# Kernel tuning notes

Hardware: AMD Instinct MI355X
Metric: run time of the kernel (lower is better)

Reference implementation:

```python
import jax, jax.numpy as jnp
import numpy as np
from jax import lax


def setup_inputs() -> dict:
    key = jax.random.key(0)
    ks = jax.random.split(key, 20)
    B, D, T = 1024, 256, 128
    H, O = 256, 64
    f32 = jnp.float32
    rn = lambda k, shape, sc: jax.random.normal(k, shape, f32) * sc
    ru = lambda k, shape: jax.random.uniform(k, shape, f32)
    return {
        "x": jax.random.normal(ks[0], (B, D, T), f32),
        "W_in": rn(ks[1], (H, D), 1.0 / np.sqrt(D)),
        "b_in": rn(ks[2], (H,), 0.02),
        "beta1": ru(ks[3], (H,)),
        "thr1": ru(ks[4], (H,)),
        "W_h": rn(ks[5], (H, H), 1.0 / np.sqrt(H)),
        "b_h": rn(ks[6], (H,), 0.02),
        "beta2": ru(ks[7], (H,)),
        "thr2": ru(ks[8], (H,)),
        "W_h1": rn(ks[9], (H, H), 1.0 / np.sqrt(H)),
        "b_h1": rn(ks[10], (H,), 0.02),
        "W_f": rn(ks[11], (O, H), 1.0 / np.sqrt(H)),
        "b_f": rn(ks[12], (O,), 0.02),
        "beta_f": ru(ks[13], (O,)),
        "W_a": rn(ks[14], (O, H), 1.0 / np.sqrt(H)),
        "b_a": rn(ks[15], (O,), 0.02),
        "beta_a": ru(ks[16], (O,)),
    }


def _spike(u):
    # heaviside(u > 0); surrogate grad only matters in backward
    return (u > 0).astype(u.dtype)


def reference(x, W_in, b_in, beta1, thr1, W_h, b_h, beta2, thr2,
              W_h1, b_h1, W_f, b_f, beta_f, W_a, b_a, beta_a):
    B = x.shape[0]
    H0, H1, H2 = W_in.shape[0], W_h.shape[0], W_h1.shape[0]
    O = W_f.shape[0]
    dt = x.dtype
    # snntorch clamps learnable beta to [0, 1] in the state update
    b1c = jnp.clip(beta1, 0.0, 1.0)
    b2c = jnp.clip(beta2, 0.0, 1.0)
    bfc = jnp.clip(beta_f, 0.0, 1.0)
    bac = jnp.clip(beta_a, 0.0, 1.0)
    xT = jnp.transpose(x, (2, 0, 1))  # [T, B, D]

    def lif(mem, cur, bc, thr):
        # snntorch Leaky, reset_mechanism='subtract': reset from PREVIOUS mem (detached)
        reset = lax.stop_gradient(_spike(mem - thr))
        mem = bc * mem + cur - reset * thr
        spk = _spike(mem - thr)
        return spk, mem

    def step(carry, xt):
        m1, m2, m3, mf, ma = carry
        cur1 = xt @ W_in.T + b_in
        s1, m1 = lif(m1, cur1, b1c, thr1)
        cur2 = s1 @ W_h.T + b_h
        s2, m2 = lif(m2, cur2, b2c, thr2)
        # source bug preserved: third layer reuses lif_hidden (beta2, thr2)
        cur3 = s2 @ W_h1.T + b_h1
        s3, m3 = lif(m3, cur3, b2c, thr2)
        # output LI neurons: reset_mechanism='none'
        mf = bfc * mf + (s3 @ W_f.T + b_f)
        ma = bac * ma + (s3 @ W_a.T + b_a)
        return (m1, m2, m3, mf, ma), None

    z = lambda n: jnp.zeros((B, n), dt)
    init = (z(H0), z(H1), z(H2), z(O), z(O))
    (m1, m2, m3, mf, ma), _ = lax.scan(step, init, xT)
    return jax.nn.sigmoid(mf), jax.nn.sigmoid(ma)
```

## Files before the change

### kernel.cpp

```cpp
#include <hip/hip_runtime.h>
#include <math.h>
#include <stdint.h>


namespace {

constexpr int Bsz = 1024;
constexpr int Dd  = 256;
constexpr int Tt  = 128;
constexpr int Hh  = 256;
constexpr int Oo  = 64;

__global__ void pack_t(const float* __restrict__ W, float* __restrict__ Wt,
                       int R, int C) {
    int idx = blockIdx.x * 256 + threadIdx.x;
    if (idx >= (C + 1) * R) return;
    int c = idx / R, r = idx - c * R;
    Wt[idx] = (c < C) ? W[(size_t)r * C + c] : 0.f;
}

__global__ void pack_o(const float* __restrict__ Wf, const float* __restrict__ Wa,
                       float* __restrict__ WtO) {
    int idx = blockIdx.x * 256 + threadIdx.x;
    if (idx >= 257 * 128) return;
    int k = idx >> 7, o = idx & 127;
    float v = 0.f;
    if (k < 256) v = (o < 64) ? Wf[(size_t)o * 256 + k] : Wa[(size_t)(o - 64) * 256 + k];
    WtO[idx] = v;
}

__device__ __forceinline__ float clamp01(float v) { return fminf(fmaxf(v, 0.f), 1.f); }

__device__ __forceinline__ bool lif_step(float& m, float cur, float B, float Th) {
    const float r = (__fsub_rn(m, Th) > 0.f) ? Th : 0.f;
    m = __fsub_rn(__fadd_rn(__fmul_rn(B, m), cur), r);
    return __fsub_rn(m, Th) > 0.f;
}

__device__ __forceinline__ void make_masks(int nib, int lane, uint64_t* M) {
    #pragma unroll
    for (int q = 0; q < 4; ++q) {
        const int v   = __shfl(nib, 16 * q + (lane >> 2), 64);
        const int bit = (v >> (lane & 3)) & 1;
        M[q] = __ballot(bit != 0);
    }
}

__device__ __forceinline__ int compact(int nib, int lane, const uint64_t* M,
                                       uint16_t* lst) {
    const int p0 = (int)__popcll(M[0]);
    const int p1 = (int)__popcll(M[1]);
    const int p2 = (int)__popcll(M[2]);
    const int p3 = (int)__popcll(M[3]);
    const int q  = lane >> 4;
    const int base = ((q >= 1) ? p0 : 0) + ((q >= 2) ? p1 : 0) + ((q >= 3) ? p2 : 0);
    const uint64_t mq = (q & 2) ? ((q & 1) ? M[3] : M[2])
                                : ((q & 1) ? M[1] : M[0]);
    const int posb = (lane & 15) << 2;
    const int r0 = base + (int)__popcll(mq & ((1ull << posb) - 1ull));
    const int s1 = nib & 1;
    const int s2 = s1 + ((nib >> 1) & 1);
    const int s3 = s2 + ((nib >> 2) & 1);
    const int nb = lane << 2;
    if (nib & 1) lst[r0]      = (uint16_t)nb;
    if (nib & 2) lst[r0 + s1] = (uint16_t)(nb + 1);
    if (nib & 4) lst[r0 + s2] = (uint16_t)(nb + 2);
    if (nib & 8) lst[r0 + s3] = (uint16_t)(nb + 3);
    const int n    = p0 + p1 + p2 + p3;
    const int npad = (n + 7) & ~7;
    if (lane < npad - n) lst[n + lane] = (uint16_t)Hh;
    return npad;
}


__device__ __forceinline__ void issue8h(const char* __restrict__ tab,
                                        uint4 I, int offB, float4* w) {
    const int k[8] = {(int)(I.x & 0xffff), (int)(I.x >> 16),
                      (int)(I.y & 0xffff), (int)(I.y >> 16),
                      (int)(I.z & 0xffff), (int)(I.z >> 16),
                      (int)(I.w & 0xffff), (int)(I.w >> 16)};
    #pragma unroll
    for (int i = 0; i < 8; ++i)
        w[i] = *(const float4*)(tab + (k[i] << 10) + offB);
}

__device__ __forceinline__ void cons8h(float4& c, const float4* w) {
    #pragma unroll
    for (int i = 0; i < 8; ++i) {
        c.x = __fadd_rn(c.x, w[i].x);
        c.y = __fadd_rn(c.y, w[i].y);
        c.z = __fadd_rn(c.z, w[i].z);
        c.w = __fadd_rn(c.w, w[i].w);
    }
}

__device__ __forceinline__ float4 sum_h(const uint16_t* lst, int nbat,
                                        const float* __restrict__ tab, int offB) {
    float4 c = {0.f, 0.f, 0.f, 0.f};
    if (nbat == 0) return c;
    const char* tb = (const char*)tab;
    float4 A[8], B[8];
    issue8h(tb, *(const uint4*)(lst), offB, A);
    int i = 1;
    for (; i + 1 < nbat; i += 2) {
        issue8h(tb, *(const uint4*)(lst + 8 * i), offB, B);
        cons8h(c, A);
        issue8h(tb, *(const uint4*)(lst + 8 * (i + 1)), offB, A);
        cons8h(c, B);
    }
    if (i < nbat) {
        issue8h(tb, *(const uint4*)(lst + 8 * i), offB, B);
        cons8h(c, A);
        cons8h(c, B);
    } else {
        cons8h(c, A);
    }
    return c;
}


__device__ __forceinline__ void issue8o(const char* __restrict__ tab,
                                        uint4 I, int offB, float2* w) {
    const int k[8] = {(int)(I.x & 0xffff), (int)(I.x >> 16),
                      (int)(I.y & 0xffff), (int)(I.y >> 16),
                      (int)(I.z & 0xffff), (int)(I.z >> 16),
                      (int)(I.w & 0xffff), (int)(I.w >> 16)};
    #pragma unroll
    for (int i = 0; i < 8; ++i)
        w[i] = *(const float2*)(tab + (k[i] << 9) + offB);
}

__device__ __forceinline__ void cons8o(float2& c, const float2* w) {
    #pragma unroll
    for (int i = 0; i < 8; ++i) {
        c.x = __fadd_rn(c.x, w[i].x);
        c.y = __fadd_rn(c.y, w[i].y);
    }
}

__device__ __forceinline__ float2 sum_o(const uint16_t* lst, int nbat,
                                        const float* __restrict__ tab, int offB) {
    float2 c = {0.f, 0.f};
    if (nbat == 0) return c;
    const char* tb = (const char*)tab;
    float2 A[8], B[8];
    issue8o(tb, *(const uint4*)(lst), offB, A);
    int i = 1;
    for (; i + 1 < nbat; i += 2) {
        issue8o(tb, *(const uint4*)(lst + 8 * i), offB, B);
        cons8o(c, A);
        issue8o(tb, *(const uint4*)(lst + 8 * (i + 1)), offB, A);
        cons8o(c, B);
    }
    if (i < nbat) {
        issue8o(tb, *(const uint4*)(lst + 8 * i), offB, B);
        cons8o(c, A);
        cons8o(c, B);
    } else {
        cons8o(c, A);
    }
    return c;
}

__global__ __launch_bounds__(256, 1) void snn_rec(
    const float* __restrict__ cur1,
    const float* __restrict__ Wt_h, const float* __restrict__ Wt_h1,
    const float* __restrict__ WtO,
    const float* __restrict__ beta1, const float* __restrict__ thr1,
    const float* __restrict__ b_h,  const float* __restrict__ beta2, const float* __restrict__ thr2,
    const float* __restrict__ b_h1,
    const float* __restrict__ b_f,  const float* __restrict__ beta_f,
    const float* __restrict__ b_a,  const float* __restrict__ beta_a,
    float* __restrict__ m1s, float* __restrict__ m2s, float* __restrict__ m3s,
    float* __restrict__ mos, float* __restrict__ out,
    int TC, int first)
{
    __shared__ __attribute__((aligned(16))) uint16_t lists[4][272];

    const int tid  = threadIdx.x;
    const int lane = tid & 63;
    const int b    = blockIdx.x * 4 + (tid >> 6);
    uint16_t* lst  = lists[tid >> 6];
    const int off4 = lane * 4;
    const int off2 = lane * 2;
    const int offBh = lane * 16;
    const int offBo = lane * 8;

    const float4 B1v  = *(const float4*)(beta1 + off4);
    const float4 Th1v = *(const float4*)(thr1  + off4);
    const float4 bhv  = *(const float4*)(b_h   + off4);
    const float4 B2v  = *(const float4*)(beta2 + off4);
    const float4 Th2v = *(const float4*)(thr2  + off4);
    const float4 bh1v = *(const float4*)(b_h1  + off4);
    const float4 B1c  = {clamp01(B1v.x), clamp01(B1v.y), clamp01(B1v.z), clamp01(B1v.w)};
    const float4 B2c  = {clamp01(B2v.x), clamp01(B2v.y), clamp01(B2v.z), clamp01(B2v.w)};

    const int oo = off2 & 63;
    const float* bop = (lane < 32) ? b_f    : b_a;
    const float* Bop = (lane < 32) ? beta_f : beta_a;
    const float bo0 = bop[oo], bo1 = bop[oo + 1];
    const float Bo0 = clamp01(Bop[oo]), Bo1 = clamp01(Bop[oo + 1]);

    float4 m1, m2, m3;
    float mo0, mo1;
    if (first) {
        m1 = m2 = m3 = make_float4(0.f, 0.f, 0.f, 0.f);
        mo0 = mo1 = 0.f;
    } else {
        m1 = *(const float4*)(m1s + (size_t)b * Hh + off4);
        m2 = *(const float4*)(m2s + (size_t)b * Hh + off4);
        m3 = *(const float4*)(m3s + (size_t)b * Hh + off4);
        const float2 mo = *(const float2*)(mos + (size_t)b * 128 + off2);
        mo0 = mo.x; mo1 = mo.y;
    }

    const float* __restrict__ curb = cur1 + (size_t)b * TC * Hh + off4;
    float4 cur = *(const float4*)(curb);
    uint64_t M[4];

    for (int t = 0; t < TC; ++t) {
        int nib = 0;
        nib |= (int)lif_step(m1.x, cur.x, B1c.x, Th1v.x);
        nib |= (int)lif_step(m1.y, cur.y, B1c.y, Th1v.y) << 1;
        nib |= (int)lif_step(m1.z, cur.z, B1c.z, Th1v.z) << 2;
        nib |= (int)lif_step(m1.w, cur.w, B1c.w, Th1v.w) << 3;
        make_masks(nib, lane, M);
        int npad = compact(nib, lane, M, lst);
        if (t + 1 < TC) cur = *(const float4*)(curb + (size_t)(t + 1) * Hh);

        float4 s = sum_h(lst, npad >> 3, Wt_h, offBh);
        nib  = (int)lif_step(m2.x, __fadd_rn(s.x, bhv.x), B2c.x, Th2v.x);
        nib |= (int)lif_step(m2.y, __fadd_rn(s.y, bhv.y), B2c.y, Th2v.y) << 1;
        nib |= (int)lif_step(m2.z, __fadd_rn(s.z, bhv.z), B2c.z, Th2v.z) << 2;
        nib |= (int)lif_step(m2.w, __fadd_rn(s.w, bhv.w), B2c.w, Th2v.w) << 3;
        make_masks(nib, lane, M);
        npad = compact(nib, lane, M, lst);

        s = sum_h(lst, npad >> 3, Wt_h1, offBh);
        nib  = (int)lif_step(m3.x, __fadd_rn(s.x, bh1v.x), B2c.x, Th2v.x);
        nib |= (int)lif_step(m3.y, __fadd_rn(s.y, bh1v.y), B2c.y, Th2v.y) << 1;
        nib |= (int)lif_step(m3.z, __fadd_rn(s.z, bh1v.z), B2c.z, Th2v.z) << 2;
        nib |= (int)lif_step(m3.w, __fadd_rn(s.w, bh1v.w), B2c.w, Th2v.w) << 3;
        make_masks(nib, lane, M);
        npad = compact(nib, lane, M, lst);

        const float2 os = sum_o(lst, npad >> 3, WtO, offBo);
        mo0 = __fadd_rn(__fmul_rn(Bo0, mo0), __fadd_rn(os.x, bo0));
        mo1 = __fadd_rn(__fmul_rn(Bo1, mo1), __fadd_rn(os.y, bo1));
    }

    *(float4*)(m1s + (size_t)b * Hh + off4) = m1;
    *(float4*)(m2s + (size_t)b * Hh + off4) = m2;
    *(float4*)(m3s + (size_t)b * Hh + off4) = m3;
    *(float2*)(mos + (size_t)b * 128 + off2) = make_float2(mo0, mo1);

    float* dst = out + ((lane < 32) ? 0 : (size_t)Bsz * Oo) + (size_t)b * Oo + oo;
    const float o0 = (float)(1.0 / (1.0 + exp(-(double)mo0)));
    const float o1 = (float)(1.0 / (1.0 + exp(-(double)mo1)));
    *(float2*)dst = make_float2(o0, o1);
}

template<int TT>
__global__ __launch_bounds__(256) void gemm_l1_lds(
    const float* __restrict__ x, const float* __restrict__ Wt_in,
    const float* __restrict__ b_in, float* __restrict__ cur1,
    int tg_base, int TCloc)
{
    __shared__ float xs[Dd][TT];
    const int h   = threadIdx.x;
    const int b   = blockIdx.x;
    const int ty  = blockIdx.y;
    const int tg0 = tg_base + ty * TT;
    const float* xb = x + (size_t)b * Dd * Tt + tg0;
    constexpr int T4 = TT / 4;
    for (int v = threadIdx.x; v < Dd * T4; v += 256) {
        const int d = v / T4, j4 = v - d * T4;
        *(float4*)&xs[d][j4 * 4] = *(const float4*)(xb + (size_t)d * Tt + j4 * 4);
    }
    __syncthreads();
    float c[TT];
    #pragma unroll
    for (int j = 0; j < TT; ++j) c[j] = 0.f;
    for (int d = 0; d < Dd; ++d) {
        const float w = Wt_in[d * Hh + h];
        #pragma unroll
        for (int j = 0; j < TT; ++j) c[j] = fmaf(w, xs[d][j], c[j]);
    }
    const float bb = b_in[h];
    float* cb = cur1 + ((size_t)b * TCloc + ty * TT) * Hh;
    #pragma unroll
    for (int j = 0; j < TT; ++j) cb[j * Hh + h] = __fadd_rn(c[j], bb);
}

template<int TT>
__global__ __launch_bounds__(256) void gemm_l1_simple(
    const float* __restrict__ x, const float* __restrict__ Wt_in,
    const float* __restrict__ b_in, float* __restrict__ cur1, int tg0)
{
    const int h = threadIdx.x;
    const int b = blockIdx.x;
    float c[TT];
    #pragma unroll
    for (int j = 0; j < TT; ++j) c[j] = 0.f;
    const float* xb = x + (size_t)b * Dd * Tt + tg0;
    for (int d = 0; d < Dd; ++d) {
        const float w = Wt_in[d * Hh + h];
        const float* xp = xb + (size_t)d * Tt;
        #pragma unroll
        for (int j = 0; j < TT; ++j) c[j] = fmaf(w, xp[j], c[j]);
    }
    const float bb = b_in[h];
    float* cb = cur1 + (size_t)b * TT * Hh;
    #pragma unroll
    for (int j = 0; j < TT; ++j) cb[j * Hh + h] = __fadd_rn(c[j], bb);
}

}

extern "C" void kernel_launch(void* const* d_in, const int* in_sizes, int n_in,
                              void* d_out, int out_size, void* d_ws, size_t ws_size,
                              hipStream_t stream) {
    const float* x      = (const float*)d_in[0];
    const float* W_in   = (const float*)d_in[1];
    const float* b_in   = (const float*)d_in[2];
    const float* beta1  = (const float*)d_in[3];
    const float* thr1   = (const float*)d_in[4];
    const float* W_h    = (const float*)d_in[5];
    const float* b_h    = (const float*)d_in[6];
    const float* beta2  = (const float*)d_in[7];
    const float* thr2   = (const float*)d_in[8];
    const float* W_h1   = (const float*)d_in[9];
    const float* b_h1   = (const float*)d_in[10];
    const float* W_f    = (const float*)d_in[11];
    const float* b_f    = (const float*)d_in[12];
    const float* beta_f = (const float*)d_in[13];
    const float* W_a    = (const float*)d_in[14];
    const float* b_a    = (const float*)d_in[15];
    const float* beta_a = (const float*)d_in[16];
    float* out = (float*)d_out;

    float* ws = (float*)d_ws;
    size_t off = 0;
    auto alloc = [&](size_t n) { float* p = ws + off; off += n; return p; };
    float* Wt_in = alloc(257 * 256);
    float* Wt_h  = alloc(257 * 256);
    float* Wt_h1 = alloc(257 * 256);
    float* WtO   = alloc(257 * 128);
    float* m1s   = alloc((size_t)Bsz * Hh);
    float* m2s   = alloc((size_t)Bsz * Hh);
    float* m3s   = alloc((size_t)Bsz * Hh);
    float* mos   = alloc((size_t)Bsz * 128);
    const size_t fixed = off;

    int TC = 1;
    const int cands[8] = {128, 64, 32, 16, 8, 4, 2, 1};
    for (int i = 0; i < 8; ++i) {
        if ((fixed + (size_t)cands[i] * Bsz * Hh) * sizeof(float) <= ws_size) { TC = cands[i]; break; }
    }
    float* cur1 = alloc((size_t)TC * Bsz * Hh);

    pack_t<<<257, 256, 0, stream>>>(W_in, Wt_in, 256, 256);
    pack_t<<<257, 256, 0, stream>>>(W_h,  Wt_h,  256, 256);
    pack_t<<<257, 256, 0, stream>>>(W_h1, Wt_h1, 256, 256);
    pack_o<<<129, 256, 0, stream>>>(W_f, W_a, WtO);

    const int nch = Tt / TC;
    for (int c = 0; c < nch; ++c) {
        const int tg = c * TC;
        if (TC >= 32)
            gemm_l1_lds<32><<<dim3(Bsz, TC / 32), 256, 0, stream>>>(x, Wt_in, b_in, cur1, tg, TC);
        else if (TC == 16)
            gemm_l1_lds<16><<<dim3(Bsz, 1), 256, 0, stream>>>(x, Wt_in, b_in, cur1, tg, TC);
        else if (TC == 8)
            gemm_l1_lds<8><<<dim3(Bsz, 1), 256, 0, stream>>>(x, Wt_in, b_in, cur1, tg, TC);
        else if (TC == 4)
            gemm_l1_simple<4><<<Bsz, 256, 0, stream>>>(x, Wt_in, b_in, cur1, tg);
        else if (TC == 2)
            gemm_l1_simple<2><<<Bsz, 256, 0, stream>>>(x, Wt_in, b_in, cur1, tg);
        else
            gemm_l1_simple<1><<<Bsz, 256, 0, stream>>>(x, Wt_in, b_in, cur1, tg);

        snn_rec<<<Bsz / 4, 256, 0, stream>>>(
            cur1, Wt_h, Wt_h1, WtO,
            beta1, thr1, b_h, beta2, thr2, b_h1,
            b_f, beta_f, b_a, beta_a,
            m1s, m2s, m3s, mos, out, TC, (c == 0) ? 1 : 0);
    }
}
```

Measured before the change: 1.352 ms.

## Split each batch row across two wavefronts and register-tile layer-1 GEMM

The recurrent SNN kernel now assigns one batch row to a 128-thread block of two wavefronts, each owning half of the hidden units. Spike masks are exchanged through shared memory with a block barrier at every layer and timestep. This doubles the number of waves working on the latency-bound sparse gather-accumulate, at the cost of three __syncthreads per step. Separately, a new layer-1 GEMM kernel gives each thread 4 hidden outputs by TT/4 timesteps in registers, so each weight float4 load is reused across several timesteps.

```diff
diff --git a/kernel.cpp b/kernel.cpp
--- a/kernel.cpp
+++ b/kernel.cpp
@@ -37,17 +37,17 @@
     return __fsub_rn(m, Th) > 0.f;
 }
 
-__device__ __forceinline__ void make_masks(int nib, int lane, uint64_t* M) {
-    #pragma unroll
-    for (int q = 0; q < 4; ++q) {
-        const int v   = __shfl(nib, 16 * q + (lane >> 2), 64);
-        const int bit = (v >> (lane & 3)) & 1;
-        M[q] = __ballot(bit != 0);
-    }
-}
-
-__device__ __forceinline__ int compact(int nib, int lane, const uint64_t* M,
-                                       uint16_t* lst) {
+__device__ __forceinline__ void make_half_masks(int nib2, int lane, uint64_t* W) {
+    #pragma unroll
+    for (int j = 0; j < 2; ++j) {
+        const int v   = __shfl(nib2, 32 * j + (lane >> 1), 64);
+        const int bit = (v >> (lane & 1)) & 1;
+        W[j] = __ballot(bit != 0);
+    }
+}
+
+__device__ __forceinline__ int compact(int lane, const uint64_t* M, uint16_t* lst) {
+    const int nib = (int)((M[lane >> 4] >> ((lane & 15) << 2)) & 0xFull);
     const int p0 = (int)__popcll(M[0]);
     const int p1 = (int)__popcll(M[1]);
     const int p2 = (int)__popcll(M[2]);
@@ -74,32 +74,30 @@
 
 
 __device__ __forceinline__ void issue8h(const char* __restrict__ tab,
-                                        uint4 I, int offB, float4* w) {
-    const int k[8] = {(int)(I.x & 0xffff), (int)(I.x >> 16),
-                      (int)(I.y & 0xffff), (int)(I.y >> 16),
-                      (int)(I.z & 0xffff), (int)(I.z >> 16),
-                      (int)(I.w & 0xffff), (int)(I.w >> 16)};
+                                        uint4 I, int offB, float2* w) {
+    const uint32_t k[8] = {(I.x & 0xffffu) << 10, (I.x >> 16) << 10,
+                           (I.y & 0xffffu) << 10, (I.y >> 16) << 10,
+                           (I.z & 0xffffu) << 10, (I.z >> 16) << 10,
+                           (I.w & 0xffffu) << 10, (I.w >> 16) << 10};
     #pragma unroll
     for (int i = 0; i < 8; ++i)
-        w[i] = *(const float4*)(tab + (k[i] << 10) + offB);
-}
-
-__device__ __forceinline__ void cons8h(float4& c, const float4* w) {
+        w[i] = *(const float2*)(tab + k[i] + offB);
+}
+
+__device__ __forceinline__ void cons8h(float2& c, const float2* w) {
     #pragma unroll
     for (int i = 0; i < 8; ++i) {
         c.x = __fadd_rn(c.x, w[i].x);
         c.y = __fadd_rn(c.y, w[i].y);
-        c.z = __fadd_rn(c.z, w[i].z);
-        c.w = __fadd_rn(c.w, w[i].w);
-    }
-}
-
-__device__ __forceinline__ float4 sum_h(const uint16_t* lst, int nbat,
+    }
+}
+
+__device__ __forceinline__ float2 sum_h(const uint16_t* lst, int nbat,
                                         const float* __restrict__ tab, int offB) {
-    float4 c = {0.f, 0.f, 0.f, 0.f};
+    float2 c = {0.f, 0.f};
     if (nbat == 0) return c;
     const char* tb = (const char*)tab;
-    float4 A[8], B[8];
+    float2 A[8], B[8];
     issue8h(tb, *(const uint4*)(lst), offB, A);
     int i = 1;
     for (; i + 1 < nbat; i += 2) {
@@ -120,30 +118,27 @@
 
 
 __device__ __forceinline__ void issue8o(const char* __restrict__ tab,
-                                        uint4 I, int offB, float2* w) {
-    const int k[8] = {(int)(I.x & 0xffff), (int)(I.x >> 16),
-                      (int)(I.y & 0xffff), (int)(I.y >> 16),
-                      (int)(I.z & 0xffff), (int)(I.z >> 16),
-                      (int)(I.w & 0xffff), (int)(I.w >> 16)};
+                                        uint4 I, int offB, float* w) {
+    const uint32_t k[8] = {(I.x & 0xffffu) << 9, (I.x >> 16) << 9,
+                           (I.y & 0xffffu) << 9, (I.y >> 16) << 9,
+                           (I.z & 0xffffu) << 9, (I.z >> 16) << 9,
+                           (I.w & 0xffffu) << 9, (I.w >> 16) << 9};
     #pragma unroll
     for (int i = 0; i < 8; ++i)
-        w[i] = *(const float2*)(tab + (k[i] << 9) + offB);
-}
-
-__device__ __forceinline__ void cons8o(float2& c, const float2* w) {
-    #pragma unroll
-    for (int i = 0; i < 8; ++i) {
-        c.x = __fadd_rn(c.x, w[i].x);
-        c.y = __fadd_rn(c.y, w[i].y);
-    }
-}
-
-__device__ __forceinline__ float2 sum_o(const uint16_t* lst, int nbat,
-                                        const float* __restrict__ tab, int offB) {
-    float2 c = {0.f, 0.f};
+        w[i] = *(const float*)(tab + k[i] + offB);
+}
+
+__device__ __forceinline__ void cons8o(float& c, const float* w) {
+    #pragma unroll
+    for (int i = 0; i < 8; ++i) c = __fadd_rn(c, w[i]);
+}
+
+__device__ __forceinline__ float sum_o(const uint16_t* lst, int nbat,
+                                       const float* __restrict__ tab, int offB) {
+    float c = 0.f;
     if (nbat == 0) return c;
     const char* tb = (const char*)tab;
-    float2 A[8], B[8];
+    float A[8], B[8];
     issue8o(tb, *(const uint4*)(lst), offB, A);
     int i = 1;
     for (; i + 1 < nbat; i += 2) {
@@ -162,7 +157,7 @@
     return c;
 }
 
-__global__ __launch_bounds__(256, 1) void snn_rec(
+__global__ __launch_bounds__(128, 2) void snn_rec(
     const float* __restrict__ cur1,
     const float* __restrict__ Wt_h, const float* __restrict__ Wt_h1,
     const float* __restrict__ WtO,
@@ -175,89 +170,144 @@
     float* __restrict__ mos, float* __restrict__ out,
     int TC, int first)
 {
-    __shared__ __attribute__((aligned(16))) uint16_t lists[4][272];
+    __shared__ __attribute__((aligned(16))) uint16_t lists[2][272];
+    __shared__ uint64_t mbuf[3][2][2];
 
     const int tid  = threadIdx.x;
     const int lane = tid & 63;
-    const int b    = blockIdx.x * 4 + (tid >> 6);
-    uint16_t* lst  = lists[tid >> 6];
-    const int off4 = lane * 4;
-    const int off2 = lane * 2;
-    const int offBh = lane * 16;
-    const int offBo = lane * 8;
-
-    const float4 B1v  = *(const float4*)(beta1 + off4);
-    const float4 Th1v = *(const float4*)(thr1  + off4);
-    const float4 bhv  = *(const float4*)(b_h   + off4);
-    const float4 B2v  = *(const float4*)(beta2 + off4);
-    const float4 Th2v = *(const float4*)(thr2  + off4);
-    const float4 bh1v = *(const float4*)(b_h1  + off4);
-    const float4 B1c  = {clamp01(B1v.x), clamp01(B1v.y), clamp01(B1v.z), clamp01(B1v.w)};
-    const float4 B2c  = {clamp01(B2v.x), clamp01(B2v.y), clamp01(B2v.z), clamp01(B2v.w)};
-
-    const int oo = off2 & 63;
-    const float* bop = (lane < 32) ? b_f    : b_a;
-    const float* Bop = (lane < 32) ? beta_f : beta_a;
-    const float bo0 = bop[oo], bo1 = bop[oo + 1];
-    const float Bo0 = clamp01(Bop[oo]), Bo1 = clamp01(Bop[oo + 1]);
-
-    float4 m1, m2, m3;
-    float mo0, mo1;
+    const int half = tid >> 6;
+    const int b    = blockIdx.x;
+    uint16_t* lst  = lists[half];
+    const int hbase = half * 128 + lane * 2;
+    const int offBh = half * 512 + lane * 8;
+    const int oslot = half * 64 + lane;
+    const int offBo = oslot * 4;
+
+    const float2 B1v  = *(const float2*)(beta1 + hbase);
+    const float2 Th1v = *(const float2*)(thr1  + hbase);
+    const float2 bhv  = *(const float2*)(b_h   + hbase);
+    const float2 B2v  = *(const float2*)(beta2 + hbase);
+    const float2 Th2v = *(const float2*)(thr2  + hbase);
+    const float2 bh1v = *(const float2*)(b_h1  + hbase);
+    const float2 B1c  = {clamp01(B1v.x), clamp01(B1v.y)};
+    const float2 B2c  = {clamp01(B2v.x), clamp01(B2v.y)};
+
+    const float* bop = half ? b_a    : b_f;
+    const float* Bop = half ? beta_a : beta_f;
+    const float bo = bop[lane];
+    const float Bo = clamp01(Bop[lane]);
+
+    float2 m1, m2, m3;
+    float mo;
     if (first) {
-        m1 = m2 = m3 = make_float4(0.f, 0.f, 0.f, 0.f);
-        mo0 = mo1 = 0.f;
+        m1 = m2 = m3 = make_float2(0.f, 0.f);
+        mo = 0.f;
     } else {
-        m1 = *(const float4*)(m1s + (size_t)b * Hh + off4);
-        m2 = *(const float4*)(m2s + (size_t)b * Hh + off4);
-        m3 = *(const float4*)(m3s + (size_t)b * Hh + off4);
-        const float2 mo = *(const float2*)(mos + (size_t)b * 128 + off2);
-        mo0 = mo.x; mo1 = mo.y;
-    }
-
-    const float* __restrict__ curb = cur1 + (size_t)b * TC * Hh + off4;
-    float4 cur = *(const float4*)(curb);
-    uint64_t M[4];
+        m1 = *(const float2*)(m1s + (size_t)b * Hh + hbase);
+        m2 = *(const float2*)(m2s + (size_t)b * Hh + hbase);
+        m3 = *(const float2*)(m3s + (size_t)b * Hh + hbase);
+        mo = mos[(size_t)b * 128 + oslot];
+    }
+
+    const float* __restrict__ curb = cur1 + (size_t)b * TC * Hh + hbase;
+    float2 cur = *(const float2*)(curb);
+    uint64_t M[4], W01[2];
 
     for (int t = 0; t < TC; ++t) {
-        int nib = 0;
-        nib |= (int)lif_step(m1.x, cur.x, B1c.x, Th1v.x);
-        nib |= (int)lif_step(m1.y, cur.y, B1c.y, Th1v.y) << 1;
-        nib |= (int)lif_step(m1.z, cur.z, B1c.z, Th1v.z) << 2;
-        nib |= (int)lif_step(m1.w, cur.w, B1c.w, Th1v.w) << 3;
-        make_masks(nib, lane, M);
-        int npad = compact(nib, lane, M, lst);
-        if (t + 1 < TC) cur = *(const float4*)(curb + (size_t)(t + 1) * Hh);
-
-        float4 s = sum_h(lst, npad >> 3, Wt_h, offBh);
-        nib  = (int)lif_step(m2.x, __fadd_rn(s.x, bhv.x), B2c.x, Th2v.x);
-        nib |= (int)lif_step(m2.y, __fadd_rn(s.y, bhv.y), B2c.y, Th2v.y) << 1;
-        nib |= (int)lif_step(m2.z, __fadd_rn(s.z, bhv.z), B2c.z, Th2v.z) << 2;
-        nib |= (int)lif_step(m2.w, __fadd_rn(s.w, bhv.w), B2c.w, Th2v.w) << 3;
-        make_masks(nib, lane, M);
-        npad = compact(nib, lane, M, lst);
+        int nib2 = 0;
+        nib2 |= (int)lif_step(m1.x, cur.x, B1c.x, Th1v.x);
+        nib2 |= (int)lif_step(m1.y, cur.y, B1c.y, Th1v.y) << 1;
+        float2 curN;
+        if (t + 1 < TC) curN = *(const float2*)(curb + (size_t)(t + 1) * Hh);
+        make_half_masks(nib2, lane, W01);
+        if (lane == 0) { mbuf[0][half][0] = W01[0]; mbuf[0][half][1] = W01[1]; }
+        __syncthreads();
+        M[0] = mbuf[0][0][0]; M[1] = mbuf[0][0][1];
+        M[2] = mbuf[0][1][0]; M[3] = mbuf[0][1][1];
+        int npad = compact(lane, M, lst);
+
+        float2 s = sum_h(lst, npad >> 3, Wt_h, offBh);
+        nib2  = (int)lif_step(m2.x, __fadd_rn(s.x, bhv.x), B2c.x, Th2v.x);
+        nib2 |= (int)lif_step(m2.y, __fadd_rn(s.y, bhv.y), B2c.y, Th2v.y) << 1;
+        make_half_masks(nib2, lane, W01);
+        if (lane == 0) { mbuf[1][half][0] = W01[0]; mbuf[1][half][1] = W01[1]; }
+        __syncthreads();
+        M[0] = mbuf[1][0][0]; M[1] = mbuf[1][0][1];
+        M[2] = mbuf[1][1][0]; M[3] = mbuf[1][1][1];
+        npad = compact(lane, M, lst);
 
         s = sum_h(lst, npad >> 3, Wt_h1, offBh);
-        nib  = (int)lif_step(m3.x, __fadd_rn(s.x, bh1v.x), B2c.x, Th2v.x);
-        nib |= (int)lif_step(m3.y, __fadd_rn(s.y, bh1v.y), B2c.y, Th2v.y) << 1;
-        nib |= (int)lif_step(m3.z, __fadd_rn(s.z, bh1v.z), B2c.z, Th2v.z) << 2;
-        nib |= (int)lif_step(m3.w, __fadd_rn(s.w, bh1v.w), B2c.w, Th2v.w) << 3;
-        make_masks(nib, lane, M);
-        npad = compact(nib, lane, M, lst);
-
-        const float2 os = sum_o(lst, npad >> 3, WtO, offBo);
-        mo0 = __fadd_rn(__fmul_rn(Bo0, mo0), __fadd_rn(os.x, bo0));
-        mo1 = __fadd_rn(__fmul_rn(Bo1, mo1), __fadd_rn(os.y, bo1));
-    }
-
-    *(float4*)(m1s + (size_t)b * Hh + off4) = m1;
-    *(float4*)(m2s + (size_t)b * Hh + off4) = m2;
-    *(float4*)(m3s + (size_t)b * Hh + off4) = m3;
-    *(float2*)(mos + (size_t)b * 128 + off2) = make_float2(mo0, mo1);
-
-    float* dst = out + ((lane < 32) ? 0 : (size_t)Bsz * Oo) + (size_t)b * Oo + oo;
-    const float o0 = (float)(1.0 / (1.0 + exp(-(double)mo0)));
-    const float o1 = (float)(1.0 / (1.0 + exp(-(double)mo1)));
-    *(float2*)dst = make_float2(o0, o1);
+        nib2  = (int)lif_step(m3.x, __fadd_rn(s.x, bh1v.x), B2c.x, Th2v.x);
+        nib2 |= (int)lif_step(m3.y, __fadd_rn(s.y, bh1v.y), B2c.y, Th2v.y) << 1;
+        make_half_masks(nib2, lane, W01);
+        if (lane == 0) { mbuf[2][half][0] = W01[0]; mbuf[2][half][1] = W01[1]; }
+        __syncthreads();
+        M[0] = mbuf[2][0][0]; M[1] = mbuf[2][0][1];
+        M[2] = mbuf[2][1][0]; M[3] = mbuf[2][1][1];
+        npad = compact(lane, M, lst);
+
+        const float os = sum_o(lst, npad >> 3, WtO, offBo);
+        mo = __fadd_rn(__fmul_rn(Bo, mo), __fadd_rn(os, bo));
+        cur = curN;
+    }
+
+    *(float2*)(m1s + (size_t)b * Hh + hbase) = m1;
+    *(float2*)(m2s + (size_t)b * Hh + hbase) = m2;
+    *(float2*)(m3s + (size_t)b * Hh + hbase) = m3;
+    mos[(size_t)b * 128 + oslot] = mo;
+
+    float* dst = out + (size_t)half * Bsz * Oo + (size_t)b * Oo + lane;
+    *dst = (float)(1.0 / (1.0 + exp(-(double)mo)));
+}
+
+template<int TT>
+__global__ __launch_bounds__(256) void gemm_l1_r8(
+    const float* __restrict__ x, const float* __restrict__ Wt_in,
+    const float* __restrict__ b_in, float* __restrict__ cur1,
+    int tg_base, int TCloc)
+{
+    __shared__ float xs[Dd][TT];
+    const int tid = threadIdx.x;
+    const int b   = blockIdx.x;
+    const int ty  = blockIdx.y;
+    const int tg0 = tg_base + ty * TT;
+    const float* xb = x + (size_t)b * Dd * Tt + tg0;
+    constexpr int T4 = TT / 4;
+    for (int v = tid; v < Dd * T4; v += 256) {
+        const int d = v / T4, j4 = v - d * T4;
+        *(float4*)&xs[d][j4 * 4] = *(const float4*)(xb + (size_t)d * Tt + j4 * 4);
+    }
+    __syncthreads();
+    constexpr int TS = TT / 4;
+    const int hq = tid & 63;
+    const int tq = tid >> 6;
+    float c0[TS], c1[TS], c2[TS], c3[TS];
+    #pragma unroll
+    for (int j = 0; j < TS; ++j) { c0[j] = 0.f; c1[j] = 0.f; c2[j] = 0.f; c3[j] = 0.f; }
+    const float* wp = Wt_in + hq * 4;
+    #pragma unroll 4
+    for (int d = 0; d < Dd; ++d) {
+        const float4 w = *(const float4*)(wp + (size_t)d * Hh);
+        #pragma unroll
+        for (int j = 0; j < TS; ++j) {
+            const float xv = xs[d][tq * TS + j];
+            c0[j] = fmaf(w.x, xv, c0[j]);
+            c1[j] = fmaf(w.y, xv, c1[j]);
+            c2[j] = fmaf(w.z, xv, c2[j]);
+            c3[j] = fmaf(w.w, xv, c3[j]);
+        }
+    }
+    const float4 bb = *(const float4*)(b_in + hq * 4);
+    float* cb = cur1 + ((size_t)b * TCloc + ty * TT + tq * TS) * Hh + hq * 4;
+    #pragma unroll
+    for (int j = 0; j < TS; ++j) {
+        float4 o;
+        o.x = __fadd_rn(c0[j], bb.x);
+        o.y = __fadd_rn(c1[j], bb.y);
+        o.z = __fadd_rn(c2[j], bb.z);
+        o.w = __fadd_rn(c3[j], bb.w);
+        *(float4*)(cb + (size_t)j * Hh) = o;
+    }
 }
 
 template<int TT>
@@ -368,7 +418,7 @@
     for (int c = 0; c < nch; ++c) {
         const int tg = c * TC;
         if (TC >= 32)
-            gemm_l1_lds<32><<<dim3(Bsz, TC / 32), 256, 0, stream>>>(x, Wt_in, b_in, cur1, tg, TC);
+            gemm_l1_r8<32><<<dim3(Bsz, TC / 32), 256, 0, stream>>>(x, Wt_in, b_in, cur1, tg, TC);
         else if (TC == 16)
             gemm_l1_lds<16><<<dim3(Bsz, 1), 256, 0, stream>>>(x, Wt_in, b_in, cur1, tg, TC);
         else if (TC == 8)
@@ -380,7 +430,7 @@
         else
             gemm_l1_simple<1><<<Bsz, 256, 0, stream>>>(x, Wt_in, b_in, cur1, tg);
 
-        snn_rec<<<Bsz / 4, 256, 0, stream>>>(
+        snn_rec<<<Bsz, 128, 0, stream>>>(
             cur1, Wt_h, Wt_h1, WtO,
             beta1, thr1, b_h, beta2, thr2, b_h1,
             b_f, beta_f, b_a, beta_a,
```

Measured after the change: 1.772 ms. 1.31x slower.
